# Kernel tuning notes

Measured on AMD Instinct MI355X. Metric: run time of the kernel, lower is better.

## Reference

```python
import jax, jax.numpy as jnp
import numpy as np

D_MODEL = 2048
HEAD_DIM = 128

def setup_inputs() -> dict:
    key = jax.random.key(0)
    ks = jax.random.split(key, 7)
    s = 1.0 / np.sqrt(D_MODEL)
    x = jax.random.normal(ks[0], (4, 4096, D_MODEL), dtype=jnp.float32)
    Wq = jax.random.uniform(ks[1], (D_MODEL, HEAD_DIM), jnp.float32, -s, s)
    bq = jax.random.uniform(ks[2], (HEAD_DIM,), jnp.float32, -s, s)
    Wk = jax.random.uniform(ks[3], (D_MODEL, HEAD_DIM), jnp.float32, -s, s)
    bk = jax.random.uniform(ks[4], (HEAD_DIM,), jnp.float32, -s, s)
    Wv = jax.random.uniform(ks[5], (D_MODEL, HEAD_DIM), jnp.float32, -s, s)
    bv = jax.random.uniform(ks[6], (HEAD_DIM,), jnp.float32, -s, s)
    return {"x": x, "Wq": Wq, "bq": bq, "Wk": Wk, "bk": bk, "Wv": Wv, "bv": bv}

def reference(x, Wq, bq, Wk, bk, Wv, bv):
    # x: [B, T, d_model]
    B, T, _ = x.shape
    q = jnp.einsum('btd,dh->bth', x, Wq) + bq  # [B,T,H]
    k = jnp.einsum('btd,dh->bth', x, Wk) + bk
    v = jnp.einsum('btd,dh->bth', x, Wv) + bv
    scores = jnp.einsum('bth,bsh->bts', q, k) / jnp.sqrt(jnp.float32(HEAD_DIM))  # [B,T,T]
    causal = jnp.tril(jnp.ones((T, T), dtype=bool))
    scores = jnp.where(causal[None], scores, -jnp.inf)
    probs = jax.nn.softmax(scores, axis=-1)
    return jnp.einsum('bts,bsh->bth', probs, v)  # [B,T,H]
```

## Files before the change

### kernel.cpp

```cpp
#include <hip/hip_runtime.h>
#include <math.h>

#define D_MODEL 2048
#define HD      128
#define NB      4
#define TT      4096
#define M_TOT   (NB * TT)
#define NCHB    80
#define CHT     16

typedef __attribute__((ext_vector_type(8))) short bf16x8;
typedef __attribute__((ext_vector_type(4))) float f32x4;

__device__ __forceinline__ ushort f2bf(float f) {
    union { float f; unsigned int u; } v; v.f = f;
    unsigned int u = v.u;
    unsigned int r = (u + 0x7FFFu + ((u >> 16) & 1u)) >> 16;
    return (ushort)r;
}

__device__ __forceinline__ void gload_lds16(const void* g, void* l) {
    __builtin_amdgcn_global_load_lds(
        (const __attribute__((address_space(1))) unsigned int*)g,
        (__attribute__((address_space(3))) unsigned int*)l, 16, 0, 0);
}

__global__ __launch_bounds__(256) void wt_kernel(
        const float* __restrict__ Wq, const float* __restrict__ Wk,
        const float* __restrict__ Wv, ushort* __restrict__ WT) {
    const int p  = blockIdx.y;
    const int k0 = blockIdx.x * 128;
    const float* W = (p == 0) ? Wq : ((p == 1) ? Wk : Wv);

    __shared__ ushort Ts[128 * 136];

    const int tid = threadIdx.x;
    for (int i = 0; i < 64; i++) {
        int c  = i * 256 + tid;
        int kk = c >> 7, n = c & 127;
        Ts[n * 136 + kk] = f2bf(W[(size_t)(k0 + kk) * 128 + n]);
    }
    __syncthreads();
    for (int i = 0; i < 8; i++) {
        int c = i * 256 + tid;
        int n = c >> 4, j = c & 15;
        *(uint4*)(WT + (size_t)p * (128 * 2048) + (size_t)n * 2048 + k0 + j * 8) =
            *(const uint4*)&Ts[n * 136 + j * 8];
    }
}

__global__ __launch_bounds__(256, 3) void proj_fused(
        const float* __restrict__ x, const ushort* __restrict__ WT,
        const float* __restrict__ bq, const float* __restrict__ bk, const float* __restrict__ bv,
        ushort* __restrict__ Qb, ushort* __restrict__ Kb, ushort* __restrict__ Vt) {
    const int bx0  = blockIdx.x;
    const int l    = (bx0 & 7) * 96 + (bx0 >> 3);
    const int row0 = (l / 3) * 64;
    const int p    = l % 3;
    const ushort* Wp   = WT + (size_t)p * (128 * 2048);
    const float*  bias = (p == 0) ? bq : ((p == 1) ? bk : bv);

    __shared__ ushort As[64 * 136];
    __shared__ ushort Bs[128 * 128];

    const int tid  = threadIdx.x;
    const int lane = tid & 63;
    const int wv   = tid >> 6;
    const int rw   = wv >> 1;
    const int cw   = wv & 1;
    const int quad = lane >> 4;
    const int ln16 = lane & 15;

    size_t  boff[8];
    ushort* bdst[8];
    for (int i = 0; i < 8; i++) {
        int c = i * 256 + tid;
        int n = c >> 4, j = c & 15;
        int kc = j ^ (n & 15);
        boff[i] = (size_t)n * 2048 + kc * 8;
        bdst[i] = &Bs[(i * 256 + wv * 64) * 8];
    }
    int arow[8], apos[8];
    for (int i = 0; i < 8; i++) {
        int c = i * 256 + tid;
        arow[i] = c >> 5;
        apos[i] = c & 31;
    }

    f32x4 acc[2][4];
    for (int m2 = 0; m2 < 2; m2++)
        for (int nt = 0; nt < 4; nt++)
            acc[m2][nt] = (f32x4){0.f, 0.f, 0.f, 0.f};

    float4 areg[8];
    for (int i = 0; i < 8; i++)
        areg[i] = *(const float4*)(x + (size_t)(row0 + arow[i]) * D_MODEL + apos[i] * 4);

    for (int k0 = 0; k0 < D_MODEL; k0 += 128) {
        __syncthreads();
        for (int i = 0; i < 8; i++)
            gload_lds16(Wp + boff[i] + k0, bdst[i]);
        for (int i = 0; i < 8; i++) {
            ushort4 o;
            o.x = f2bf(areg[i].x); o.y = f2bf(areg[i].y);
            o.z = f2bf(areg[i].z); o.w = f2bf(areg[i].w);
            *(ushort4*)&As[arow[i] * 136 + apos[i] * 4] = o;
        }
        __syncthreads();
        if (k0 + 128 < D_MODEL)
            for (int i = 0; i < 8; i++)
                areg[i] = *(const float4*)(x + (size_t)(row0 + arow[i]) * D_MODEL
                                             + k0 + 128 + apos[i] * 4);

        for (int mi = 0; mi < 4; mi++) {
            bf16x8 a[2], b[4];
            for (int m2 = 0; m2 < 2; m2++)
                a[m2] = *(const bf16x8*)&As[(rw * 32 + m2 * 16 + ln16) * 136 + mi * 32 + quad * 8];
            for (int nt = 0; nt < 4; nt++) {
                int n = cw * 64 + nt * 16 + ln16;
                int slot = (mi * 4 + quad) ^ (n & 15);
                b[nt] = *(const bf16x8*)&Bs[n * 128 + slot * 8];
            }
            for (int m2 = 0; m2 < 2; m2++)
                for (int nt = 0; nt < 4; nt++)
                    acc[m2][nt] = __builtin_amdgcn_mfma_f32_16x16x32_bf16(a[m2], b[nt], acc[m2][nt], 0, 0, 0);
        }
    }

    for (int nt = 0; nt < 4; nt++) {
        int h  = cw * 64 + nt * 16 + ln16;
        float bc = bias[h];
        for (int m2 = 0; m2 < 2; m2++) {
            int rbase = row0 + rw * 32 + m2 * 16 + quad * 4;
            if (p < 2) {
                ushort* O = (p == 0) ? Qb : Kb;
                for (int r = 0; r < 4; r++)
                    O[(size_t)(rbase + r) * HD + h] = f2bf(acc[m2][nt][r] + bc);
            } else {
                int b = rbase >> 12;
                int t = rbase & 4095;
                ushort4 o;
                o.x = f2bf(acc[m2][nt][0] + bc);
                o.y = f2bf(acc[m2][nt][1] + bc);
                o.z = f2bf(acc[m2][nt][2] + bc);
                o.w = f2bf(acc[m2][nt][3] + bc);
                *(ushort4*)(Vt + ((size_t)b * HD + h) * TT + t) = o;
            }
        }
    }
}

#define SCALE2 0.12751744573223862f

__global__ __launch_bounds__(512, 4) void attn_part(
        const ushort* __restrict__ Qb, const ushort* __restrict__ Kb,
        const ushort* __restrict__ Vt, float* __restrict__ Opart,
        float* __restrict__ Mpart, float* __restrict__ Lpart) {
    const int blk = blockIdx.x;
    const int bb  = blk & 3;
    const int cid = blk >> 2;

    int rem = cid, qt2 = 31;
    for (;;) {
        int cnt = (2 * qt2 + 17) >> 4;
        if (rem < cnt) break;
        rem -= cnt; --qt2;
    }
    const int ch    = rem;
    const int st_lo = ch * CHT;
    const int st_hi = min(2 * qt2 + 2, st_lo + CHT);
    const int q0    = qt2 * 128;

    __shared__ ushort Ks[2][64 * 128];
    __shared__ ushort Vs[2][128 * 64];
    __shared__ ushort Ps[128 * 64];

    const int tid  = threadIdx.x;
    const int lane = tid & 63;
    const int wv   = tid >> 6;
    const int quad = lane >> 4;
    const int ln16 = lane & 15;
    const int sw8  = ln16 & 7;

    int koff[2], voff[2], ldso[2];
    for (int i = 0; i < 2; i++) {
        int c = i * 512 + tid;
        { int r = c >> 4, j = c & 15, kc = j ^ (r & 15);
          koff[i] = r * HD + kc * 8; }
        { int h = c >> 3, j = c & 7, kc = j ^ (h & 7);
          voff[i] = h * TT + kc * 8; }
        ldso[i] = (i * 512 + wv * 64) * 8;
    }
    const ushort* kbase = Kb + (size_t)bb * TT * HD;
    const ushort* vbase = Vt + (size_t)bb * HD * TT;

    {
        const int s0 = st_lo * 64;
        for (int i = 0; i < 2; i++) gload_lds16(kbase + (size_t)s0 * HD + koff[i], &Ks[0][ldso[i]]);
        for (int i = 0; i < 2; i++) gload_lds16(vbase + s0 + voff[i], &Vs[0][ldso[i]]);
    }
    bf16x8 qf[4];
    {
        const ushort* qrow = Qb + (size_t)(bb * TT + q0 + 16 * wv + ln16) * HD;
        for (int kc = 0; kc < 4; kc++)
            qf[kc] = *(const bf16x8*)(qrow + kc * 32 + quad * 8);
    }

    f32x4 o_acc[8];
    for (int nt = 0; nt < 8; nt++) o_acc[nt] = (f32x4){0.f, 0.f, 0.f, 0.f};
    float lsum[4];
    for (int r = 0; r < 4; r++) lsum[r] = 0.f;

    __syncthreads();

    for (int st = st_lo; st < st_hi; st++) {
        const int s0  = st * 64;
        const int buf = (st - st_lo) & 1;

        if (st + 1 < st_hi) {
            const int s1 = s0 + 64;
            for (int i = 0; i < 2; i++) gload_lds16(kbase + (size_t)s1 * HD + koff[i], &Ks[buf ^ 1][ldso[i]]);
            for (int i = 0; i < 2; i++) gload_lds16(vbase + s1 + voff[i], &Vs[buf ^ 1][ldso[i]]);
        }

        f32x4 sacc[4];
        for (int nt = 0; nt < 4; nt++) sacc[nt] = (f32x4){0.f, 0.f, 0.f, 0.f};
        for (int kc = 0; kc < 4; kc++) {
            int lc = kc * 4 + quad;
            for (int nt = 0; nt < 4; nt++) {
                int r = nt * 16 + ln16;
                bf16x8 b = *(const bf16x8*)&Ks[buf][r * 128 + ((lc ^ ln16) * 8)];
                sacc[nt] = __builtin_amdgcn_mfma_f32_16x16x32_bf16(qf[kc], b, sacc[nt], 0, 0, 0);
            }
        }

        const bool diag = (st >= 2 * qt2);
        for (int r = 0; r < 4; r++) {
            for (int nt = 0; nt < 4; nt++) {
                float s = sacc[nt][r] * SCALE2;
                if (diag) {
                    int sg = s0 + nt * 16 + ln16;
                    int qg = q0 + 16 * wv + quad * 4 + r;
                    if (sg > qg) s = -INFINITY;
                }
                float pv = exp2f(s);
                sacc[nt][r] = pv;
                lsum[r] += pv;
            }
        }

        for (int nt = 0; nt < 4; nt++)
            for (int r = 0; r < 4; r++) {
                int row = 16 * wv + quad * 4 + r;
                int cj  = nt * 2 + (ln16 >> 3);
                Ps[row * 64 + ((cj ^ (row & 7)) * 8) + sw8] = f2bf(sacc[nt][r]);
            }

        for (int kc2 = 0; kc2 < 2; kc2++) {
            int lc = kc2 * 4 + quad;
            int prow = 16 * wv + ln16;
            bf16x8 a = *(const bf16x8*)&Ps[prow * 64 + ((lc ^ sw8) * 8)];
            for (int nt = 0; nt < 8; nt++) {
                int h = nt * 16 + ln16;
                bf16x8 b = *(const bf16x8*)&Vs[buf][h * 64 + ((lc ^ sw8) * 8)];
                o_acc[nt] = __builtin_amdgcn_mfma_f32_16x16x32_bf16(a, b, o_acc[nt], 0, 0, 0);
            }
        }

        __syncthreads();
    }

    for (int off = 8; off >= 1; off >>= 1)
        for (int r = 0; r < 4; r++)
            lsum[r] += __shfl_xor(lsum[r], off);

    const size_t slot = (size_t)bb * NCHB + cid;
    for (int nt = 0; nt < 8; nt++)
        for (int r = 0; r < 4; r++)
            Opart[(slot * 128 + 16 * wv + quad * 4 + r) * HD + nt * 16 + ln16] = o_acc[nt][r];
    if (ln16 == 0)
        for (int r = 0; r < 4; r++) {
            Mpart[slot * 128 + 16 * wv + quad * 4 + r] = 0.f;
            Lpart[slot * 128 + 16 * wv + quad * 4 + r] = lsum[r];
        }
}

__global__ __launch_bounds__(256) void merge_kernel(
        const float* __restrict__ Opart, const float* __restrict__ Mpart,
        const float* __restrict__ Lpart, float* __restrict__ out) {
    const int qt  = blockIdx.x;
    const int bb  = blockIdx.y;
    const int qt2 = qt >> 1;
    const int rh  = (qt & 1) * 64;
    const int nch = (2 * qt2 + 17) >> 4;
    int base = 0;
    for (int j = 31; j > qt2; --j) base += (2 * j + 17) >> 4;

    const int tid = threadIdx.x;
    const int q0  = qt * 64;
    for (int e = tid; e < 64 * 32; e += 256) {
        int row = e >> 5;
        int c4  = e & 31;
        int srow = rh + row;
        float M = -INFINITY;
        float mv[4];
        for (int ch = 0; ch < nch; ch++) {
            mv[ch] = Mpart[((size_t)bb * NCHB + base + ch) * 128 + srow];
            M = fmaxf(M, mv[ch]);
        }
        float L = 0.f;
        float w[4];
        for (int ch = 0; ch < nch; ch++) {
            w[ch] = __expf(mv[ch] - M);
            L += w[ch] * Lpart[((size_t)bb * NCHB + base + ch) * 128 + srow];
        }
        float4 acc = {0.f, 0.f, 0.f, 0.f};
        for (int ch = 0; ch < nch; ch++) {
            const float4 o = *(const float4*)(Opart +
                (((size_t)bb * NCHB + base + ch) * 128 + srow) * HD + c4 * 4);
            acc.x += w[ch] * o.x; acc.y += w[ch] * o.y;
            acc.z += w[ch] * o.z; acc.w += w[ch] * o.w;
        }
        float invL = 1.f / L;
        float4 res = {acc.x * invL, acc.y * invL, acc.z * invL, acc.w * invL};
        *(float4*)(out + ((size_t)bb * TT + q0 + row) * HD + c4 * 4) = res;
    }
}

extern "C" void kernel_launch(void* const* d_in, const int* in_sizes, int n_in,
                              void* d_out, int out_size, void* d_ws, size_t ws_size,
                              hipStream_t stream) {
    const float* x  = (const float*)d_in[0];
    const float* Wq = (const float*)d_in[1];
    const float* bq = (const float*)d_in[2];
    const float* Wk = (const float*)d_in[3];
    const float* bk = (const float*)d_in[4];
    const float* Wv = (const float*)d_in[5];
    const float* bv = (const float*)d_in[6];
    float* out = (float*)d_out;

    ushort* WT = (ushort*)d_ws;
    ushort* Qb = WT + (size_t)3 * HD * D_MODEL;
    ushort* Kb = Qb + (size_t)M_TOT * HD;
    ushort* Vt = Kb + (size_t)M_TOT * HD;
    float* Opart = (float*)(Vt + (size_t)M_TOT * HD);
    float* Mpart = Opart + (size_t)NB * NCHB * 128 * HD;
    float* Lpart = Mpart + (size_t)NB * NCHB * 128;

    hipLaunchKernelGGL(wt_kernel, dim3(16, 3), dim3(256), 0, stream, Wq, Wk, Wv, WT);
    hipLaunchKernelGGL(proj_fused, dim3(768), dim3(256), 0, stream,
                       x, WT, bq, bk, bv, Qb, Kb, Vt);
    hipLaunchKernelGGL(attn_part, dim3(NB * NCHB), dim3(512), 0, stream,
                       Qb, Kb, Vt, Opart, Mpart, Lpart);
    hipLaunchKernelGGL(merge_kernel, dim3(64, NB), dim3(256), 0, stream,
                       Opart, Mpart, Lpart, out);
}
```

Baseline: 296.9 us.

## Double-buffer weight tiles in projection GEMM and swizzle A tile in LDS

The projection kernel now double-buffers the bf16 weight tile in LDS, issuing the next tile's async global-to-LDS loads before running the MFMA loop on the current tile, so the load latency overlaps compute. The padded A tile (stride 136) is replaced by an unpadded XOR-swizzled layout to avoid bank conflicts without padding. The larger LDS footprint lowers the launch-bounds occupancy target from 3 to 2 blocks per CU, which may reduce latency hiding from concurrent blocks.

```diff
diff --git a/kernel.cpp b/kernel.cpp
--- a/kernel.cpp
+++ b/kernel.cpp
@@ -49,7 +49,7 @@
     }
 }
 
-__global__ __launch_bounds__(256, 3) void proj_fused(
+__global__ __launch_bounds__(256, 2) void proj_fused(
         const float* __restrict__ x, const ushort* __restrict__ WT,
         const float* __restrict__ bq, const float* __restrict__ bk, const float* __restrict__ bv,
         ushort* __restrict__ Qb, ushort* __restrict__ Kb, ushort* __restrict__ Vt) {
@@ -60,8 +60,8 @@
     const ushort* Wp   = WT + (size_t)p * (128 * 2048);
     const float*  bias = (p == 0) ? bq : ((p == 1) ? bk : bv);
 
-    __shared__ ushort As[64 * 136];
-    __shared__ ushort Bs[128 * 128];
+    __shared__ ushort As[64 * 128];
+    __shared__ ushort Bs[2][128 * 128];
 
     const int tid  = threadIdx.x;
     const int lane = tid & 63;
@@ -71,14 +71,14 @@
     const int quad = lane >> 4;
     const int ln16 = lane & 15;
 
-    size_t  boff[8];
-    ushort* bdst[8];
+    size_t boff[8];
+    int    bdo[8];
     for (int i = 0; i < 8; i++) {
         int c = i * 256 + tid;
         int n = c >> 4, j = c & 15;
         int kc = j ^ (n & 15);
         boff[i] = (size_t)n * 2048 + kc * 8;
-        bdst[i] = &Bs[(i * 256 + wv * 64) * 8];
+        bdo[i]  = (i * 256 + wv * 64) * 8;
     }
     int arow[8], apos[8];
     for (int i = 0; i < 8; i++) {
@@ -95,36 +95,56 @@
     float4 areg[8];
     for (int i = 0; i < 8; i++)
         areg[i] = *(const float4*)(x + (size_t)(row0 + arow[i]) * D_MODEL + apos[i] * 4);
-
+    for (int i = 0; i < 8; i++)
+        gload_lds16(Wp + boff[i], &Bs[0][bdo[i]]);
+    __syncthreads();
+    for (int i = 0; i < 8; i++) {
+        ushort4 o;
+        o.x = f2bf(areg[i].x); o.y = f2bf(areg[i].y);
+        o.z = f2bf(areg[i].z); o.w = f2bf(areg[i].w);
+        *(ushort4*)&As[arow[i] * 128 + (((apos[i] >> 1) ^ (arow[i] & 15)) * 8)
+                       + (apos[i] & 1) * 4] = o;
+    }
+    __syncthreads();
+
+    int cur = 0;
     for (int k0 = 0; k0 < D_MODEL; k0 += 128) {
-        __syncthreads();
-        for (int i = 0; i < 8; i++)
-            gload_lds16(Wp + boff[i] + k0, bdst[i]);
-        for (int i = 0; i < 8; i++) {
-            ushort4 o;
-            o.x = f2bf(areg[i].x); o.y = f2bf(areg[i].y);
-            o.z = f2bf(areg[i].z); o.w = f2bf(areg[i].w);
-            *(ushort4*)&As[arow[i] * 136 + apos[i] * 4] = o;
-        }
-        __syncthreads();
-        if (k0 + 128 < D_MODEL)
+        const bool pf = (k0 + 128 < D_MODEL);
+        if (pf) {
+            for (int i = 0; i < 8; i++)
+                gload_lds16(Wp + boff[i] + k0 + 128, &Bs[cur ^ 1][bdo[i]]);
             for (int i = 0; i < 8; i++)
                 areg[i] = *(const float4*)(x + (size_t)(row0 + arow[i]) * D_MODEL
                                              + k0 + 128 + apos[i] * 4);
+        }
 
         for (int mi = 0; mi < 4; mi++) {
             bf16x8 a[2], b[4];
-            for (int m2 = 0; m2 < 2; m2++)
-                a[m2] = *(const bf16x8*)&As[(rw * 32 + m2 * 16 + ln16) * 136 + mi * 32 + quad * 8];
+            for (int m2 = 0; m2 < 2; m2++) {
+                int r = rw * 32 + m2 * 16 + ln16;
+                a[m2] = *(const bf16x8*)&As[r * 128 + (((mi * 4 + quad) ^ ln16) * 8)];
+            }
             for (int nt = 0; nt < 4; nt++) {
                 int n = cw * 64 + nt * 16 + ln16;
                 int slot = (mi * 4 + quad) ^ (n & 15);
-                b[nt] = *(const bf16x8*)&Bs[n * 128 + slot * 8];
+                b[nt] = *(const bf16x8*)&Bs[cur][n * 128 + slot * 8];
             }
             for (int m2 = 0; m2 < 2; m2++)
                 for (int nt = 0; nt < 4; nt++)
                     acc[m2][nt] = __builtin_amdgcn_mfma_f32_16x16x32_bf16(a[m2], b[nt], acc[m2][nt], 0, 0, 0);
         }
+
+        __syncthreads();
+        if (pf)
+            for (int i = 0; i < 8; i++) {
+                ushort4 o;
+                o.x = f2bf(areg[i].x); o.y = f2bf(areg[i].y);
+                o.z = f2bf(areg[i].z); o.w = f2bf(areg[i].w);
+                *(ushort4*)&As[arow[i] * 128 + (((apos[i] >> 1) ^ (arow[i] & 15)) * 8)
+                               + (apos[i] & 1) * 4] = o;
+            }
+        __syncthreads();
+        cur ^= 1;
     }
 
     for (int nt = 0; nt < 4; nt++) {
```

Result: slower. 313.6 us (+5.6%).
